# Optimization experiments

Hardware: AMD Instinct MI355X
Metric: run time of the kernel (lower is better)

The kernel has to match this reference:

```python
import jax, jax.numpy as jnp
import numpy as np

N = 50000

def _norm_coeffs(edge_index, n):
    # add self-loops, compute symmetric GCN normalization D^-1/2 (A+I) D^-1/2
    loops = jnp.arange(n, dtype=edge_index.dtype)
    src = jnp.concatenate([edge_index[0], loops])
    dst = jnp.concatenate([edge_index[1], loops])
    deg = jax.ops.segment_sum(jnp.ones_like(dst, dtype=jnp.float32), dst, num_segments=n)
    dinv = jnp.where(deg > 0, jax.lax.rsqrt(deg), 0.0)
    norm = dinv[src] * dinv[dst]  # [E+N]
    return src, dst, norm

def _gcn(x, W, b, src, dst, norm, n):
    h = x @ W                                   # [N, out]
    m = h[src] * norm[:, None]                  # [E+N, out] gather + scale
    return jax.ops.segment_sum(m, dst, num_segments=n) + b

def setup_inputs() -> dict:
    key = jax.random.key(0)
    ks = jax.random.split(key, 8)
    d, h = 96, 96
    E = 800000
    return {
        "x": jax.random.normal(ks[0], (N, d), jnp.float32),
        "edge_index": jax.random.randint(ks[1], (2, E), 0, N, dtype=jnp.int64),
        "h_prev": jax.random.normal(ks[2], (N, h), jnp.float32),
        "Wx": jax.random.normal(ks[3], (d, h), jnp.float32) * (1.0 / np.sqrt(d)),
        "bx": jnp.zeros((h,), jnp.float32),
        "Wuh": jax.random.normal(ks[4], (2 * h, h), jnp.float32) * (1.0 / np.sqrt(2 * h)),
        "buh": jnp.zeros((h,), jnp.float32),
        "Wch": jax.random.normal(ks[5], (2 * h, h), jnp.float32) * (1.0 / np.sqrt(2 * h)),
        "bch": jnp.zeros((h,), jnp.float32),
    }

def reference(x, edge_index, h_prev, Wx, bx, Wuh, buh, Wch, bch):
    n = x.shape[0]
    src, dst, norm = _norm_coeffs(edge_index, n)
    x_gcn = _gcn(x, Wx, bx, src, dst, norm, n)
    combined = jnp.concatenate([x_gcn, h_prev], axis=1)
    # original computes gcn_uh(combined) twice for u and r; identical math -> compute once
    g = jax.nn.sigmoid(_gcn(combined, Wuh, buh, src, dst, norm, n))
    u = g
    r = g
    combined_r = jnp.concatenate([x_gcn, r * h_prev], axis=1)
    c = jnp.tanh(_gcn(combined_r, Wch, bch, src, dst, norm, n))
    return u * h_prev + (1.0 - u) * c
```

## Files before the change

### kernel.cpp

```cpp
#include <hip/hip_runtime.h>
#include <hip/hip_bf16.h>

#define D 96
#define CAP 64
typedef long long i64;
typedef unsigned short u16;

typedef __bf16 bf16x8 __attribute__((ext_vector_type(8)));
typedef float f32x4 __attribute__((ext_vector_type(4)));

__device__ __forceinline__ float bf2f(u16 u) {
  union { unsigned u; float f; } x; x.u = ((unsigned)u) << 16; return x.f;
}
__device__ __forceinline__ void unpack8(uint4 p, float* a) {
  a[0] = bf2f((u16)(p.x & 0xffff)); a[1] = bf2f((u16)(p.x >> 16));
  a[2] = bf2f((u16)(p.y & 0xffff)); a[3] = bf2f((u16)(p.y >> 16));
  a[4] = bf2f((u16)(p.z & 0xffff)); a[5] = bf2f((u16)(p.z >> 16));
  a[6] = bf2f((u16)(p.w & 0xffff)); a[7] = bf2f((u16)(p.w >> 16));
}

__device__ __forceinline__ void split8(const float* v8, bf16x8& hi, bf16x8& lo) {
  unsigned hu[4], lu[4];
#pragma unroll
  for (int p = 0; p < 4; p++) {
    float v0 = v8[2 * p], v1 = v8[2 * p + 1];
    unsigned u0 = __float_as_uint(v0), u1 = __float_as_uint(v1);
    hu[p] = (u0 >> 16) | (u1 & 0xffff0000u);
    float l0 = v0 - __uint_as_float(u0 & 0xffff0000u);
    float l1 = v1 - __uint_as_float(u1 & 0xffff0000u);
    lu[p] = (__float_as_uint(l0) >> 16) | (__float_as_uint(l1) & 0xffff0000u);
  }
  union { uint4 q; bf16x8 v; } H, L;
  H.q = make_uint4(hu[0], hu[1], hu[2], hu[3]);
  L.q = make_uint4(lu[0], lu[1], lu[2], lu[3]);
  hi = H.v; lo = L.v;
}

__global__ __launch_bounds__(256) void k_detect(const unsigned* __restrict__ w,
                                                int* flag, int E) {
  if (threadIdx.x < 64) {
    int lane = threadIdx.x;
    int lim = (E < 2048) ? E : 2048;
    unsigned acc = 0;
    for (int j = lane; j < lim; j += 64) acc |= w[2 * j + 1];
#pragma unroll
    for (int off = 32; off > 0; off >>= 1) acc |= __shfl_down(acc, off, 64);
    if (lane == 0) *flag = (acc == 0) ? 1 : 0;
  }
}

__global__ __launch_bounds__(256) void k_wprep(const float* __restrict__ Wx,
                                               const float* __restrict__ Wuh,
                                               const float* __restrict__ Wch,
                                               u16* __restrict__ wxh, u16* __restrict__ wxl,
                                               u16* __restrict__ wuhh, u16* __restrict__ wuhl,
                                               u16* __restrict__ wchh, u16* __restrict__ wchl) {
  int cid = blockIdx.x * 256 + threadIdx.x;
  const float* W; u16 *oh, *ol; int loc;
  if (cid < 1152) { W = Wx; oh = wxh; ol = wxl; loc = cid; }
  else if (cid < 3456) { W = Wuh; oh = wuhh; ol = wuhl; loc = cid - 1152; }
  else if (cid < 5760) { W = Wch; oh = wchh; ol = wchl; loc = cid - 3456; }
  else return;
  int oct = loc / 96;
  int j = loc - oct * 96;
  int k0 = oct * 8;
  unsigned hu[4], lu[4];
#pragma unroll
  for (int p = 0; p < 4; p++) {
    float v0 = W[(size_t)(k0 + 2 * p) * D + j];
    float v1 = W[(size_t)(k0 + 2 * p + 1) * D + j];
    unsigned u0 = __float_as_uint(v0), u1 = __float_as_uint(v1);
    hu[p] = (u0 >> 16) | (u1 & 0xffff0000u);
    float l0 = v0 - __uint_as_float(u0 & 0xffff0000u);
    float l1 = v1 - __uint_as_float(u1 & 0xffff0000u);
    lu[p] = (__float_as_uint(l0) >> 16) | (__float_as_uint(l1) & 0xffff0000u);
  }
  *(uint4*)&oh[(size_t)loc * 8] = make_uint4(hu[0], hu[1], hu[2], hu[3]);
  *(uint4*)&ol[(size_t)loc * 8] = make_uint4(lu[0], lu[1], lu[2], lu[3]);
}

__global__ __launch_bounds__(256) void k_bucket(const int* __restrict__ e32,
                                                const i64* __restrict__ e64,
                                                const int* __restrict__ flagp,
                                                uint2* __restrict__ region,
                                                int* __restrict__ cntmat,
                                                int E, int N, int NB) {
  __shared__ int lofs[256];
  const int tid = threadIdx.x;
  const int blk = blockIdx.x;
  lofs[tid] = 0;
  __syncthreads();
  const int f = *flagp;
  const int chunk = (E + gridDim.x - 1) / gridDim.x;
  const int lo = blk * chunk;
  const int hi = min(E, lo + chunk);
  for (int i = lo + tid; i < hi; i += 256) {
    int d, s;
    if (f) { d = (int)e64[(size_t)E + i]; s = (int)e64[i]; }
    else   { d = e32[(size_t)E + i];      s = e32[i]; }
    if ((unsigned)d >= (unsigned)N || (unsigned)s >= (unsigned)N) continue;
    int q = d >> 8;
    int r = atomicAdd(&lofs[q], 1);
    if (r < CAP)
      region[((size_t)q * 256 + blk) * CAP + r] = make_uint2((unsigned)s, (unsigned)d);
  }
  __syncthreads();
  if (tid < NB) cntmat[blk * 256 + tid] = min(lofs[tid], CAP);
}

__global__ __launch_bounds__(256) void k_csr(const uint2* __restrict__ region,
                                             const int* __restrict__ cntmat,
                                             int* __restrict__ deg,
                                             int* __restrict__ csrp, int NB) {
  __shared__ int ldeg[256];
  __shared__ int lcsr[256 * CAP];
  const int tid = threadIdx.x;
  const int b = blockIdx.x;
  ldeg[tid] = 0;
  __syncthreads();
  int cnt = cntmat[tid * 256 + b];
  const uint2* cell = region + ((size_t)b * 256 + tid) * CAP;
  for (int k = 0; k < cnt; k++) {
    uint2 e = cell[k];
    int node = (int)(e.y & 255u);
    int r = atomicAdd(&ldeg[node], 1);
    if (r < CAP) lcsr[node * CAP + r] = (int)e.x;
  }
  __syncthreads();
  deg[(b << 8) + tid] = ldeg[tid];
  const uint4* src = (const uint4*)lcsr;
  uint4* dst = (uint4*)(csrp + ((size_t)b << 8) * CAP);
#pragma unroll
  for (int it = 0; it < (256 * CAP) / 4 / 256; it++)
    dst[tid + it * 256] = src[tid + it * 256];
}

template <int KTOT, int MODE>
__global__ __launch_bounds__(128) void gemm_mfma(
    const float* __restrict__ xin, const float* __restrict__ xg,
    const float* __restrict__ hprev, const float* __restrict__ gmul,
    const u16* __restrict__ whi, const u16* __restrict__ wlo,
    const int* __restrict__ deg, __hip_bfloat16* __restrict__ t, int N) {
  constexpr bool KS = (KTOT == 192);
  __shared__ float lcomb[64][25];
  const int l = threadIdx.x & 63;
  const int wv = threadIdx.x >> 6;
  const int j16 = l & 15;
  const int koct = l >> 4;
  const int rb = KS ? blockIdx.x * 16 : blockIdx.x * 32 + wv * 16;
  const int row = rb + j16;
  const bool rok = row < N;

  f32x4 c0, c1, c2, c3, c4, c5;
#pragma unroll
  for (int i = 0; i < 4; i++) { c0[i] = 0.f; c1[i] = 0.f; c2[i] = 0.f;
                                c3[i] = 0.f; c4[i] = 0.f; c5[i] = 0.f; }

#define COLT(CT, ACC) do {                                                  \
    union { uint4 q; bf16x8 v; } Bh, Bl;                                    \
    const size_t wb = (so + (CT)*16 + j16) * 8;                             \
    Bh.q = *(const uint4*)&whi[wb];                                         \
    Bl.q = *(const uint4*)&wlo[wb];                                         \
    ACC = __builtin_amdgcn_mfma_f32_16x16x32_bf16(ah, Bh.v, ACC, 0, 0, 0);  \
    ACC = __builtin_amdgcn_mfma_f32_16x16x32_bf16(al, Bh.v, ACC, 0, 0, 0);  \
    ACC = __builtin_amdgcn_mfma_f32_16x16x32_bf16(ah, Bl.v, ACC, 0, 0, 0);  \
  } while (0)

#pragma unroll
  for (int ss = 0; ss < 3; ss++) {
    const int s = KS ? (wv * 3 + ss) : ss;
    float a8[8] = {0.f, 0.f, 0.f, 0.f, 0.f, 0.f, 0.f, 0.f};
    if (rok) {
      const int kb = ss * 32 + koct * 8;
      const float* src;
      if (MODE == 0) src = xin;
      else if (!KS || wv == 0) src = xg;
      else src = hprev;
      float4 va = *(const float4*)&src[(size_t)row * D + kb];
      float4 vb = *(const float4*)&src[(size_t)row * D + kb + 4];
      if (MODE == 2 && KS && wv == 1) {
        float4 ga = *(const float4*)&gmul[(size_t)row * D + kb];
        float4 gb = *(const float4*)&gmul[(size_t)row * D + kb + 4];
        va.x *= ga.x; va.y *= ga.y; va.z *= ga.z; va.w *= ga.w;
        vb.x *= gb.x; vb.y *= gb.y; vb.z *= gb.z; vb.w *= gb.w;
      }
      a8[0] = va.x; a8[1] = va.y; a8[2] = va.z; a8[3] = va.w;
      a8[4] = vb.x; a8[5] = vb.y; a8[6] = vb.z; a8[7] = vb.w;
    }
    bf16x8 ah, al;
    split8(a8, ah, al);
    const size_t so = (size_t)(s * 4 + koct) * 96;
    COLT(0, c0); COLT(1, c1); COLT(2, c2);
    COLT(3, c3); COLT(4, c4); COLT(5, c5);
  }
#undef COLT

  if (KS) {
    if (wv == 1) {
#pragma unroll
      for (int r = 0; r < 4; r++) {
        lcomb[l][0 + r]  = c0[r]; lcomb[l][4 + r]  = c1[r];
        lcomb[l][8 + r]  = c2[r]; lcomb[l][12 + r] = c3[r];
        lcomb[l][16 + r] = c4[r]; lcomb[l][20 + r] = c5[r];
      }
    }
    __syncthreads();
    if (wv == 1) return;
#pragma unroll
    for (int r = 0; r < 4; r++) {
      c0[r] += lcomb[l][0 + r];  c1[r] += lcomb[l][4 + r];
      c2[r] += lcomb[l][8 + r];  c3[r] += lcomb[l][12 + r];
      c4[r] += lcomb[l][16 + r]; c5[r] += lcomb[l][20 + r];
    }
  }

  const int r0 = rb + koct * 4;
  float dv[4];
#pragma unroll
  for (int r = 0; r < 4; r++)
    dv[r] = (r0 + r < N) ? rsqrtf((float)deg[r0 + r] + 1.0f) : 0.f;
#pragma unroll
  for (int r = 0; r < 4; r++) {
    int orow = r0 + r;
    if (orow >= N) continue;
    __hip_bfloat16* tp = &t[(size_t)orow * D + j16];
    tp[0]  = __float2bfloat16(c0[r] * dv[r]);
    tp[16] = __float2bfloat16(c1[r] * dv[r]);
    tp[32] = __float2bfloat16(c2[r] * dv[r]);
    tp[48] = __float2bfloat16(c3[r] * dv[r]);
    tp[64] = __float2bfloat16(c4[r] * dv[r]);
    tp[80] = __float2bfloat16(c5[r] * dv[r]);
  }
}

template <int MODE>
__global__ __launch_bounds__(192) void gather_fin(
    const __hip_bfloat16* __restrict__ t, const int* __restrict__ deg,
    const int* __restrict__ csrp,
    const float* __restrict__ bias,
    const float* __restrict__ g, const float* __restrict__ hprev,
    float* __restrict__ outf, int N) {
  __shared__ int lidx[16 * 65];
  __shared__ int ldeg[16];
  const int tid = threadIdx.x;
  const int vbase = blockIdx.x * 16;
#pragma unroll
  for (int it = 0; it < 6; it++) {
    int i = tid + it * 192;
    if (i < 1024) {
      int n = i >> 6, j = i & 63;
      lidx[n * 65 + j] = csrp[((size_t)(vbase + n)) * CAP + j];
    }
  }
  if (tid < 16) ldeg[tid] = deg[vbase + tid];
  __syncthreads();
  const int n = tid / 12;
  const int c8 = tid - n * 12;
  const int v = vbase + n;
  if (v >= N) return;
  const uint4* t8 = (const uint4*)t;
  float acc[8];
  unpack8(t8[(size_t)v * 12 + c8], acc);
  int dv_i = ldeg[n];
  int nb = min(dv_i, CAP);
  const int* ip = &lidx[n * 65];
  int j = 0;
  for (; j + 8 <= nb; j += 8) {
    int s0 = ip[j],     s1 = ip[j + 1], s2 = ip[j + 2], s3 = ip[j + 3];
    int s4 = ip[j + 4], s5 = ip[j + 5], s6 = ip[j + 6], s7 = ip[j + 7];
    uint4 p0 = t8[(size_t)s0 * 12 + c8];
    uint4 p1 = t8[(size_t)s1 * 12 + c8];
    uint4 p2 = t8[(size_t)s2 * 12 + c8];
    uint4 p3 = t8[(size_t)s3 * 12 + c8];
    uint4 p4 = t8[(size_t)s4 * 12 + c8];
    uint4 p5 = t8[(size_t)s5 * 12 + c8];
    uint4 p6 = t8[(size_t)s6 * 12 + c8];
    uint4 p7 = t8[(size_t)s7 * 12 + c8];
    float a0[8], a1[8], a2[8], a3[8], a4[8], a5[8], a6[8], a7[8];
    unpack8(p0, a0); unpack8(p1, a1); unpack8(p2, a2); unpack8(p3, a3);
    unpack8(p4, a4); unpack8(p5, a5); unpack8(p6, a6); unpack8(p7, a7);
#pragma unroll
    for (int q = 0; q < 8; q++)
      acc[q] += ((a0[q] + a1[q]) + (a2[q] + a3[q])) + ((a4[q] + a5[q]) + (a6[q] + a7[q]));
  }
  for (; j + 4 <= nb; j += 4) {
    int s0 = ip[j], s1 = ip[j + 1], s2 = ip[j + 2], s3 = ip[j + 3];
    uint4 p0 = t8[(size_t)s0 * 12 + c8];
    uint4 p1 = t8[(size_t)s1 * 12 + c8];
    uint4 p2 = t8[(size_t)s2 * 12 + c8];
    uint4 p3 = t8[(size_t)s3 * 12 + c8];
    float a0[8], a1[8], a2[8], a3[8];
    unpack8(p0, a0); unpack8(p1, a1); unpack8(p2, a2); unpack8(p3, a3);
#pragma unroll
    for (int q = 0; q < 8; q++) acc[q] += (a0[q] + a1[q]) + (a2[q] + a3[q]);
  }
  for (; j < nb; j++) {
    int s = ip[j];
    float a0[8];
    unpack8(t8[(size_t)s * 12 + c8], a0);
#pragma unroll
    for (int q = 0; q < 8; q++) acc[q] += a0[q];
  }
  float dv = rsqrtf((float)dv_i + 1.0f);
  float4 bA = ((const float4*)bias)[c8 * 2];
  float4 bB = ((const float4*)bias)[c8 * 2 + 1];
  float z[8] = {dv * acc[0] + bA.x, dv * acc[1] + bA.y, dv * acc[2] + bA.z, dv * acc[3] + bA.w,
                dv * acc[4] + bB.x, dv * acc[5] + bB.y, dv * acc[6] + bB.z, dv * acc[7] + bB.w};
  const size_t oidx = (size_t)v * 12 + c8;
  float4 oA, oB;
  if (MODE == 1) {
    oA = make_float4(z[0], z[1], z[2], z[3]);
    oB = make_float4(z[4], z[5], z[6], z[7]);
  } else if (MODE == 2) {
    oA = make_float4(1.0f / (1.0f + expf(-z[0])), 1.0f / (1.0f + expf(-z[1])),
                     1.0f / (1.0f + expf(-z[2])), 1.0f / (1.0f + expf(-z[3])));
    oB = make_float4(1.0f / (1.0f + expf(-z[4])), 1.0f / (1.0f + expf(-z[5])),
                     1.0f / (1.0f + expf(-z[6])), 1.0f / (1.0f + expf(-z[7])));
  } else {
    float4 uA = ((const float4*)g)[oidx * 2], uB = ((const float4*)g)[oidx * 2 + 1];
    float4 hA = ((const float4*)hprev)[oidx * 2], hB = ((const float4*)hprev)[oidx * 2 + 1];
    oA = make_float4(uA.x * hA.x + (1.0f - uA.x) * tanhf(z[0]),
                     uA.y * hA.y + (1.0f - uA.y) * tanhf(z[1]),
                     uA.z * hA.z + (1.0f - uA.z) * tanhf(z[2]),
                     uA.w * hA.w + (1.0f - uA.w) * tanhf(z[3]));
    oB = make_float4(uB.x * hB.x + (1.0f - uB.x) * tanhf(z[4]),
                     uB.y * hB.y + (1.0f - uB.y) * tanhf(z[5]),
                     uB.z * hB.z + (1.0f - uB.z) * tanhf(z[6]),
                     uB.w * hB.w + (1.0f - uB.w) * tanhf(z[7]));
  }
  ((float4*)outf)[oidx * 2] = oA;
  ((float4*)outf)[oidx * 2 + 1] = oB;
}

extern "C" void kernel_launch(void* const* d_in, const int* in_sizes, int n_in,
                              void* d_out, int out_size, void* d_ws, size_t ws_size,
                              hipStream_t stream) {
  const float* x = (const float*)d_in[0];
  const int* ei32 = (const int*)d_in[1];
  const i64* ei64 = (const i64*)d_in[1];
  const unsigned* eiw = (const unsigned*)d_in[1];
  const float* hp = (const float*)d_in[2];
  const float* Wx = (const float*)d_in[3];
  const float* bx = (const float*)d_in[4];
  const float* Wuh = (const float*)d_in[5];
  const float* buh = (const float*)d_in[6];
  const float* Wch = (const float*)d_in[7];
  const float* bch = (const float*)d_in[8];
  float* out = (float*)d_out;

  const int N = in_sizes[0] / D;
  const int E = in_sizes[1] / 2;
  const size_t NF = (size_t)N * D;
  const int NB = (N + 255) >> 8;
  const int R = NB << 8;

  char* base = (char*)d_ws;
  int* flag = (int*)base;
  u16* wxh = (u16*)(base + 256);
  u16* wxl = wxh + 9216;
  u16* wuhh = wxl + 9216;
  u16* wuhl = wuhh + 18432;
  u16* wchh = wuhl + 18432;
  u16* wchl = wchh + 18432;
  int* deg = (int*)(wchl + 18432);
  int* cntmat = deg + R;
  uint2* region = (uint2*)(cntmat + 65536);
  int* csrp = (int*)(region + (size_t)NB * 256 * CAP);
  __hip_bfloat16* t = (__hip_bfloat16*)(csrp + (size_t)R * CAP);
  float* xg = (float*)((char*)t + NF * 2);
  float* g = xg + NF;

  const int gb16 = (N + 15) / 16;
  const int gb32 = (N + 31) / 32;
  const int fb = (N + 15) / 16;

  k_detect<<<1, 256, 0, stream>>>(eiw, flag, E);
  k_wprep<<<23, 256, 0, stream>>>(Wx, Wuh, Wch, wxh, wxl, wuhh, wuhl, wchh, wchl);
  k_bucket<<<256, 256, 0, stream>>>(ei32, ei64, flag, region, cntmat, E, N, NB);
  k_csr<<<NB, 256, 0, stream>>>(region, cntmat, deg, csrp, NB);

  gemm_mfma<96, 0><<<gb32, 128, 0, stream>>>(x, nullptr, nullptr, nullptr, wxh, wxl, deg, t, N);
  gather_fin<1><<<fb, 192, 0, stream>>>(t, deg, csrp, bx, nullptr, nullptr, xg, N);

  gemm_mfma<192, 1><<<gb16, 128, 0, stream>>>(nullptr, xg, hp, nullptr, wuhh, wuhl, deg, t, N);
  gather_fin<2><<<fb, 192, 0, stream>>>(t, deg, csrp, buh, nullptr, nullptr, g, N);

  gemm_mfma<192, 2><<<gb16, 128, 0, stream>>>(nullptr, xg, hp, g, wchh, wchl, deg, t, N);
  gather_fin<3><<<fb, 192, 0, stream>>>(t, deg, csrp, bch, g, hp, out, N);
}
```

Before: 264.7 us.

## Merge setup kernels and sort gather neighbors by source-range bucket

Folds edge-dtype detection, weight bf16 splitting and edge bucketing into one launch: each bucketing block recomputes the int64 flag itself and extra blocks do the weight prep. In gather_fin, each node's neighbor list is reordered in shared memory into three source-index ranges, so gathers from nearby rows of t are issued together and may get better cache locality. The reorder adds shared-memory atomics and extra barriers to every gather launch, and every bucketing block now repeats the flag scan.

Measured after the change: 264.7 us. Within noise of the previous version (-0.0%).

```diff
diff --git a/kernel.cpp b/kernel.cpp
--- a/kernel.cpp
+++ b/kernel.cpp
@@ -36,62 +36,65 @@
   hi = H.v; lo = L.v;
 }
 
-__global__ __launch_bounds__(256) void k_detect(const unsigned* __restrict__ w,
-                                                int* flag, int E) {
-  if (threadIdx.x < 64) {
-    int lane = threadIdx.x;
+__global__ __launch_bounds__(256) void k_build(
+    const int* __restrict__ e32, const i64* __restrict__ e64,
+    const unsigned* __restrict__ eiw,
+    const float* __restrict__ Wx, const float* __restrict__ Wuh,
+    const float* __restrict__ Wch,
+    u16* __restrict__ wxh, u16* __restrict__ wxl,
+    u16* __restrict__ wuhh, u16* __restrict__ wuhl,
+    u16* __restrict__ wchh, u16* __restrict__ wchl,
+    uint2* __restrict__ region, int* __restrict__ cntmat,
+    int E, int N, int NB) {
+  const int tid = threadIdx.x;
+  if (blockIdx.x >= 256) {
+    int cid = (blockIdx.x - 256) * 256 + tid;
+    const float* W; u16 *oh, *ol; int loc;
+    if (cid < 1152) { W = Wx; oh = wxh; ol = wxl; loc = cid; }
+    else if (cid < 3456) { W = Wuh; oh = wuhh; ol = wuhl; loc = cid - 1152; }
+    else if (cid < 5760) { W = Wch; oh = wchh; ol = wchl; loc = cid - 3456; }
+    else return;
+    int oct = loc / 96;
+    int j = loc - oct * 96;
+    int k0 = oct * 8;
+    unsigned hu[4], lu[4];
+#pragma unroll
+    for (int p = 0; p < 4; p++) {
+      float v0 = W[(size_t)(k0 + 2 * p) * D + j];
+      float v1 = W[(size_t)(k0 + 2 * p + 1) * D + j];
+      unsigned u0 = __float_as_uint(v0), u1 = __float_as_uint(v1);
+      hu[p] = (u0 >> 16) | (u1 & 0xffff0000u);
+      float l0 = v0 - __uint_as_float(u0 & 0xffff0000u);
+      float l1 = v1 - __uint_as_float(u1 & 0xffff0000u);
+      lu[p] = (__float_as_uint(l0) >> 16) | (__float_as_uint(l1) & 0xffff0000u);
+    }
+    *(uint4*)&oh[(size_t)loc * 8] = make_uint4(hu[0], hu[1], hu[2], hu[3]);
+    *(uint4*)&ol[(size_t)loc * 8] = make_uint4(lu[0], lu[1], lu[2], lu[3]);
+    return;
+  }
+  __shared__ unsigned fsh[256];
+  __shared__ int lofs[256];
+  {
+    unsigned a = 0;
     int lim = (E < 2048) ? E : 2048;
-    unsigned acc = 0;
-    for (int j = lane; j < lim; j += 64) acc |= w[2 * j + 1];
-#pragma unroll
-    for (int off = 32; off > 0; off >>= 1) acc |= __shfl_down(acc, off, 64);
-    if (lane == 0) *flag = (acc == 0) ? 1 : 0;
-  }
-}
-
-__global__ __launch_bounds__(256) void k_wprep(const float* __restrict__ Wx,
-                                               const float* __restrict__ Wuh,
-                                               const float* __restrict__ Wch,
-                                               u16* __restrict__ wxh, u16* __restrict__ wxl,
-                                               u16* __restrict__ wuhh, u16* __restrict__ wuhl,
-                                               u16* __restrict__ wchh, u16* __restrict__ wchl) {
-  int cid = blockIdx.x * 256 + threadIdx.x;
-  const float* W; u16 *oh, *ol; int loc;
-  if (cid < 1152) { W = Wx; oh = wxh; ol = wxl; loc = cid; }
-  else if (cid < 3456) { W = Wuh; oh = wuhh; ol = wuhl; loc = cid - 1152; }
-  else if (cid < 5760) { W = Wch; oh = wchh; ol = wchl; loc = cid - 3456; }
-  else return;
-  int oct = loc / 96;
-  int j = loc - oct * 96;
-  int k0 = oct * 8;
-  unsigned hu[4], lu[4];
-#pragma unroll
-  for (int p = 0; p < 4; p++) {
-    float v0 = W[(size_t)(k0 + 2 * p) * D + j];
-    float v1 = W[(size_t)(k0 + 2 * p + 1) * D + j];
-    unsigned u0 = __float_as_uint(v0), u1 = __float_as_uint(v1);
-    hu[p] = (u0 >> 16) | (u1 & 0xffff0000u);
-    float l0 = v0 - __uint_as_float(u0 & 0xffff0000u);
-    float l1 = v1 - __uint_as_float(u1 & 0xffff0000u);
-    lu[p] = (__float_as_uint(l0) >> 16) | (__float_as_uint(l1) & 0xffff0000u);
-  }
-  *(uint4*)&oh[(size_t)loc * 8] = make_uint4(hu[0], hu[1], hu[2], hu[3]);
-  *(uint4*)&ol[(size_t)loc * 8] = make_uint4(lu[0], lu[1], lu[2], lu[3]);
-}
-
-__global__ __launch_bounds__(256) void k_bucket(const int* __restrict__ e32,
-                                                const i64* __restrict__ e64,
-                                                const int* __restrict__ flagp,
-                                                uint2* __restrict__ region,
-                                                int* __restrict__ cntmat,
-                                                int E, int N, int NB) {
-  __shared__ int lofs[256];
-  const int tid = threadIdx.x;
+    for (int j = tid; j < lim; j += 256) a |= eiw[2 * j + 1];
+    fsh[tid] = a;
+    __syncthreads();
+    if (tid < 128) fsh[tid] |= fsh[tid + 128];
+    __syncthreads();
+    if (tid < 64) {
+      unsigned b = fsh[tid] | fsh[tid + 64];
+#pragma unroll
+      for (int off = 32; off > 0; off >>= 1) b |= __shfl_down(b, off, 64);
+      if (tid == 0) fsh[0] = b;
+    }
+    __syncthreads();
+  }
+  const int f = (fsh[0] == 0) ? 1 : 0;
+  lofs[tid] = 0;
+  __syncthreads();
   const int blk = blockIdx.x;
-  lofs[tid] = 0;
-  __syncthreads();
-  const int f = *flagp;
-  const int chunk = (E + gridDim.x - 1) / gridDim.x;
+  const int chunk = (E + 255) / 256;
   const int lo = blk * chunk;
   const int hi = min(E, lo + chunk);
   for (int i = lo + tid; i < hi; i += 256) {
@@ -239,8 +242,12 @@
     const int* __restrict__ csrp,
     const float* __restrict__ bias,
     const float* __restrict__ g, const float* __restrict__ hprev,
-    float* __restrict__ outf, int N) {
+    float* __restrict__ outf, int N, int n1, int n2) {
   __shared__ int lidx[16 * 65];
+  __shared__ int lsort[16 * 65];
+  __shared__ int lcnt[16][4];
+  __shared__ int lbase[16][4];
+  __shared__ int lpl[16][4];
   __shared__ int ldeg[16];
   const int tid = threadIdx.x;
   const int vbase = blockIdx.x * 16;
@@ -253,17 +260,39 @@
     }
   }
   if (tid < 16) ldeg[tid] = deg[vbase + tid];
+  if (tid >= 96 && tid < 160) {
+    int n = (tid - 96) >> 2, s = (tid - 96) & 3;
+    lcnt[n][s] = 0; lpl[n][s] = 0;
+  }
   __syncthreads();
   const int n = tid / 12;
   const int c8 = tid - n * 12;
   const int v = vbase + n;
-  if (v >= N) return;
+  const int nb = min(ldeg[n], CAP);
+  for (int j = c8; j < nb; j += 12) {
+    int s = lidx[n * 65 + j];
+    int sg = (s >= n1) + (s >= n2);
+    atomicAdd(&lcnt[n][sg], 1);
+  }
+  __syncthreads();
+  if (tid < 16) {
+    lbase[tid][0] = 0;
+    lbase[tid][1] = lcnt[tid][0];
+    lbase[tid][2] = lcnt[tid][0] + lcnt[tid][1];
+  }
+  __syncthreads();
+  for (int j = c8; j < nb; j += 12) {
+    int s = lidx[n * 65 + j];
+    int sg = (s >= n1) + (s >= n2);
+    int r = atomicAdd(&lpl[n][sg], 1);
+    lsort[n * 65 + lbase[n][sg] + r] = s;
+  }
+  __syncthreads();
+
   const uint4* t8 = (const uint4*)t;
-  float acc[8];
-  unpack8(t8[(size_t)v * 12 + c8], acc);
-  int dv_i = ldeg[n];
-  int nb = min(dv_i, CAP);
-  const int* ip = &lidx[n * 65];
+  float acc[8] = {0.f, 0.f, 0.f, 0.f, 0.f, 0.f, 0.f, 0.f};
+  if (v < N) unpack8(t8[(size_t)v * 12 + c8], acc);
+  const int* ip = &lsort[n * 65];
   int j = 0;
   for (; j + 8 <= nb; j += 8) {
     int s0 = ip[j],     s1 = ip[j + 1], s2 = ip[j + 2], s3 = ip[j + 3];
@@ -301,7 +330,8 @@
 #pragma unroll
     for (int q = 0; q < 8; q++) acc[q] += a0[q];
   }
-  float dv = rsqrtf((float)dv_i + 1.0f);
+  if (v >= N) return;
+  float dv = rsqrtf((float)ldeg[n] + 1.0f);
   float4 bA = ((const float4*)bias)[c8 * 2];
   float4 bB = ((const float4*)bias)[c8 * 2 + 1];
   float z[8] = {dv * acc[0] + bA.x, dv * acc[1] + bA.y, dv * acc[2] + bA.z, dv * acc[3] + bA.w,
@@ -353,9 +383,9 @@
   const size_t NF = (size_t)N * D;
   const int NB = (N + 255) >> 8;
   const int R = NB << 8;
+  const int n1 = N / 3, n2 = 2 * (N / 3);
 
   char* base = (char*)d_ws;
-  int* flag = (int*)base;
   u16* wxh = (u16*)(base + 256);
   u16* wxl = wxh + 9216;
   u16* wuhh = wxl + 9216;
@@ -374,17 +404,17 @@
   const int gb32 = (N + 31) / 32;
   const int fb = (N + 15) / 16;
 
-  k_detect<<<1, 256, 0, stream>>>(eiw, flag, E);
-  k_wprep<<<23, 256, 0, stream>>>(Wx, Wuh, Wch, wxh, wxl, wuhh, wuhl, wchh, wchl);
-  k_bucket<<<256, 256, 0, stream>>>(ei32, ei64, flag, region, cntmat, E, N, NB);
+  k_build<<<279, 256, 0, stream>>>(ei32, ei64, eiw, Wx, Wuh, Wch,
+                                   wxh, wxl, wuhh, wuhl, wchh, wchl,
+                                   region, cntmat, E, N, NB);
   k_csr<<<NB, 256, 0, stream>>>(region, cntmat, deg, csrp, NB);
 
   gemm_mfma<96, 0><<<gb32, 128, 0, stream>>>(x, nullptr, nullptr, nullptr, wxh, wxl, deg, t, N);
-  gather_fin<1><<<fb, 192, 0, stream>>>(t, deg, csrp, bx, nullptr, nullptr, xg, N);
+  gather_fin<1><<<fb, 192, 0, stream>>>(t, deg, csrp, bx, nullptr, nullptr, xg, N, n1, n2);
 
   gemm_mfma<192, 1><<<gb16, 128, 0, stream>>>(nullptr, xg, hp, nullptr, wuhh, wuhl, deg, t, N);
-  gather_fin<2><<<fb, 192, 0, stream>>>(t, deg, csrp, buh, nullptr, nullptr, g, N);
+  gather_fin<2><<<fb, 192, 0, stream>>>(t, deg, csrp, buh, nullptr, nullptr, g, N, n1, n2);
 
   gemm_mfma<192, 2><<<gb16, 128, 0, stream>>>(nullptr, xg, hp, g, wchh, wchl, deg, t, N);
-  gather_fin<3><<<fb, 192, 0, stream>>>(t, deg, csrp, bch, g, hp, out, N);
-}
+  gather_fin<3><<<fb, 192, 0, stream>>>(t, deg, csrp, bch, g, hp, out, N, n1, n2);
+}
```
